# Optimization experiments

Measured on AMD Instinct MI355X. Metric: run time of the kernel, lower is better.

## Reference

```python
import jax, jax.numpy as jnp
import numpy as np

D_MODEL = 128
N_HEADS = 8
N_POINTS = 8
MAX_RES = 10.0


def setup_inputs() -> dict:
    key = jax.random.key(0)
    ks = jax.random.split(key, 12)
    B, C, H, W = 4, D_MODEL, 128, 128
    nh, P = N_HEADS, N_POINTS
    inp = {
        'nbr_fea': jax.random.normal(ks[0], (B, C, H, W), jnp.float32),
        'ext_fea': jax.random.normal(ks[1], (B, C, H, W), jnp.float32),
        'flow': jax.random.normal(ks[2], (B, 2, H, W), jnp.float32) * 2.0,
        'W_off': jax.random.normal(ks[3], (C, nh * P * 2), jnp.float32) * 0.02,
        'b_off': jax.random.normal(ks[4], (nh * P * 2,), jnp.float32) * 0.02,
        'W_attn': jax.random.normal(ks[5], (C, nh * P), jnp.float32) * 0.02,
        'b_attn': jnp.zeros((nh * P,), jnp.float32),
        'W_val': jax.random.normal(ks[6], (C, C), jnp.float32) * (1.0 / np.sqrt(C)),
        'b_val': jnp.zeros((C,), jnp.float32),
        'W_out': jax.random.normal(ks[7], (C, C), jnp.float32) * (1.0 / np.sqrt(C)),
        'b_out': jnp.zeros((C,), jnp.float32),
    }
    return inp


def _bilinear_gather(value, loc, H, W):
    # value: (B, nh, HW, dh)  loc: (B, nh, Q, P, 2) normalized to [0,1]
    # grid_sample semantics: align_corners=False, zero padding
    B, nh, HW, dh = value.shape
    Q, P = loc.shape[2], loc.shape[3]
    x = loc[..., 0] * W - 0.5  # (B,nh,Q,P) pixel coords
    y = loc[..., 1] * H - 0.5
    x0 = jnp.floor(x)
    y0 = jnp.floor(y)
    wx = x - x0
    wy = y - y0
    out = jnp.zeros((B, nh, Q * P, dh), value.dtype)
    for dx, dy, wgt in ((0, 0, (1 - wx) * (1 - wy)), (1, 0, wx * (1 - wy)),
                        (0, 1, (1 - wx) * wy), (1, 1, wx * wy)):
        xi = x0 + dx
        yi = y0 + dy
        valid = (xi >= 0) & (xi < W) & (yi >= 0) & (yi < H)
        xi_c = jnp.clip(xi, 0, W - 1).astype(jnp.int32)
        yi_c = jnp.clip(yi, 0, H - 1).astype(jnp.int32)
        idx = (yi_c * W + xi_c).reshape(B, nh, Q * P, 1)
        g = jnp.take_along_axis(value, idx, axis=2)  # (B,nh,QP,dh)
        w_eff = (wgt * valid.astype(value.dtype)).reshape(B, nh, Q * P, 1)
        out = out + g * w_eff
    return out.reshape(B, nh, Q, P, dh)


def reference(nbr_fea, ext_fea, flow, W_off, b_off, W_attn, b_attn, W_val, b_val, W_out, b_out):
    B, C, H, W = nbr_fea.shape
    nh, P = N_HEADS, N_POINTS
    dh = C // nh
    Q = H * W
    # normalized reference points (pixel centers / extent)
    ys = (jnp.arange(H, dtype=jnp.float32) + 0.5) / H
    xs = (jnp.arange(W, dtype=jnp.float32) + 0.5) / W
    yy, xx = jnp.meshgrid(ys, xs, indexing='ij')
    ref = jnp.stack([xx, yy], -1).reshape(Q, 2)  # (Q,2)

    ext = ext_fea.transpose(0, 2, 3, 1).reshape(B, Q, C)
    # flow-guided sampling offsets (pixels), residue bounded by tanh
    off = MAX_RES * jnp.tanh(ext @ W_off + b_off)
    off = off.reshape(B, Q, nh, P, 2)
    flow_q = flow.transpose(0, 2, 3, 1).reshape(B, Q, 1, 1, 2)
    norm = jnp.array([W, H], jnp.float32)
    loc = ref[None, :, None, None, :] + (flow_q + off) / norm  # (B,Q,nh,P,2)

    attn = jax.nn.softmax((ext @ W_attn + b_attn).reshape(B, Q, nh, P), axis=-1)

    val = (nbr_fea.transpose(0, 2, 3, 1).reshape(B, Q, C) @ W_val + b_val)
    val = val.reshape(B, Q, nh, dh).transpose(0, 2, 1, 3)  # (B,nh,HW,dh)

    sampled = _bilinear_gather(val, loc.transpose(0, 2, 1, 3, 4), H, W)  # (B,nh,Q,P,dh)
    agg = jnp.einsum('bnqpd,bqnp->bqnd', sampled, attn).reshape(B, Q, C)
    out = agg @ W_out + b_out  # (B,Q,C)
    return out.reshape(B, H, W, C).transpose(0, 3, 1, 2)
```

## Files before the change

kernel.cpp:

```cpp
#include <hip/hip_runtime.h>
#include <math.h>

namespace {
constexpr int B   = 4;
constexpr int C   = 128;
constexpr int H   = 128;
constexpr int W   = 128;
constexpr int HWn = H * W;
constexpr int NH  = 8;
}

using short8 = __attribute__((ext_vector_type(8))) short;
using f32x4  = __attribute__((ext_vector_type(4))) float;

__device__ __forceinline__ float fast_tanh(float x) {
  float e = __expf(2.f * x);
  return 1.f - 2.f / (e + 1.f);
}
__device__ __forceinline__ unsigned f2bf(float f) {
  unsigned u = __float_as_uint(f);
  return (u + 0x7FFFu + ((u >> 16) & 1u)) >> 16;
}
__device__ __forceinline__ unsigned pack2bf(float a, float b) {
  return f2bf(a) | (f2bf(b) << 16);
}

__global__ __launch_bounds__(256) void prep_weights_kernel(
    const float* __restrict__ Woff, const float* __restrict__ Wattn,
    const float* __restrict__ Wval, const float* __restrict__ Wout,
    unsigned short* __restrict__ wcat_t, unsigned short* __restrict__ wval_t,
    unsigned short* __restrict__ wout_t) {
  int row = blockIdx.x * 256 + threadIdx.x;
  if (row >= 448) return;
  const float* src; int ldn; int col; unsigned short* dst;
  if (row < 192) {
    if (row < 128) { src = Woff; ldn = 128; col = row; }
    else           { src = Wattn; ldn = 64; col = row - 128; }
    dst = wcat_t + row * 128;
  } else if (row < 320) {
    src = Wval; ldn = 128; col = row - 192; dst = wval_t + (row - 192) * 128;
  } else {
    src = Wout; ldn = 128; col = row - 320; dst = wout_t + (row - 320) * 128;
  }
  for (int k0 = 0; k0 < 128; k0 += 8) {
    unsigned pk[4];
#pragma unroll
    for (int j = 0; j < 4; ++j)
      pk[j] = pack2bf(src[(k0 + 2 * j) * ldn + col],
                      src[(k0 + 2 * j + 1) * ldn + col]);
    *(uint4*)(dst + k0) = make_uint4(pk[0], pk[1], pk[2], pk[3]);
  }
}

__global__ __launch_bounds__(256) void gemm_kernel(
    const float* __restrict__ nbr,
    const unsigned short* __restrict__ wval_t,
    const float* __restrict__ bv,
    unsigned short* __restrict__ val) {
  __shared__ unsigned short a_s[32 * 152];
  const int t    = threadIdx.x;
  const int id   = blockIdx.x;
  const int b    = id >> 9;
  const int q0   = (id & 511) * 32;
  const int wv   = t >> 6;
  const int lane = t & 63;
  const int li   = lane & 15, quad = lane >> 4;

  const float* Ab = nbr + (size_t)b * C * HWn + q0;
#pragma unroll
  for (int it = 0; it < 2; ++it) {
    int idx = t + 256 * it;
    int kp  = idx >> 3;
    int q4  = (idx & 7) * 4;
    float4 fa = *(const float4*)(Ab + (size_t)(2 * kp) * HWn + q4);
    float4 fb = *(const float4*)(Ab + (size_t)(2 * kp + 1) * HWn + q4);
    const float* pa = &fa.x; const float* pb = &fb.x;
#pragma unroll
    for (int j = 0; j < 4; ++j)
      *(unsigned*)&a_s[(q4 + j) * 152 + 2 * kp] = pack2bf(pa[j], pb[j]);
  }
  __syncthreads();

  const int mt = wv & 1;
  const int ng = (wv >> 1) * 4;
  f32x4 acc[4];
#pragma unroll
  for (int i = 0; i < 4; ++i) acc[i] = (f32x4){0.f, 0.f, 0.f, 0.f};

#pragma unroll 1
  for (int ck = 0; ck < 4; ++ck) {
    short8 af = *(const short8*)&a_s[(16 * mt + li) * 152 + ck * 32 + quad * 8];
#pragma unroll
    for (int i = 0; i < 4; ++i) {
      short8 bfr = *(const short8*)(wval_t + (size_t)(16 * (ng + i) + li) * 128 +
                                    ck * 32 + quad * 8);
      acc[i] = __builtin_amdgcn_mfma_f32_16x16x32_bf16(af, bfr, acc[i], 0, 0, 0);
    }
  }
  __syncthreads();

#pragma unroll
  for (int i = 0; i < 4; ++i) {
    int c = 16 * (ng + i) + li;
    float bias = bv[c];
#pragma unroll
    for (int reg = 0; reg < 4; ++reg) {
      int q = mt * 16 + quad * 4 + reg;
      a_s[q * 152 + c] = (unsigned short)f2bf(acc[i][reg] + bias);
    }
  }
  __syncthreads();

  {
    const int qi = t & 31, hs = t >> 5;
    uint4 v0 = *(const uint4*)&a_s[qi * 152 + 16 * hs];
    uint4 v1 = *(const uint4*)&a_s[qi * 152 + 16 * hs + 8];
    unsigned short* d = val + ((size_t)(b * NH + hs) * HWn + q0 + qi) * 16;
    *(uint4*)d = v0; *(uint4*)(d + 8) = v1;
  }
}

__global__ __launch_bounds__(256) void gather_out_kernel(
    const float* __restrict__ flow, const float* __restrict__ ext,
    const unsigned short* __restrict__ wcat_t,
    const float* __restrict__ boff, const float* __restrict__ battn,
    const unsigned short* __restrict__ val,
    const unsigned short* __restrict__ wout_t, const float* __restrict__ bout,
    float* __restrict__ out) {
  __shared__ float smem[32 * 196];
  unsigned short* a_ext = (unsigned short*)smem;
  float* l_s = smem;
  unsigned short* a_s2 = (unsigned short*)smem;
  float* c_s = smem;

  const int t  = threadIdx.x;
  const int qi = t & 31;
  const int r  = t >> 5;

  const int blk  = blockIdx.x;
  const int lin  = (blk & 7) * 256 + (blk >> 3);
  const int b    = lin >> 9;
  const int tile = lin & 511;
  const int x0   = (tile & 7) * 16;
  const int y0   = (tile >> 3) * 2;
  const int x    = x0 + (qi & 15);
  const int y    = y0 + (qi >> 4);

  const int lane = t & 63;
  const int li   = lane & 15, quad = lane >> 4;
  const int wv   = t >> 6;

  {
    const float* Eb = ext + (size_t)b * C * HWn;
#pragma unroll
    for (int it = 0; it < 2; ++it) {
      int idx = t + 256 * it;
      int kp  = idx >> 3;
      int pg  = idx & 7;
      int py  = pg >> 2;
      int xo  = (pg & 3) * 4;
      const float* src = Eb + (size_t)(2 * kp) * HWn + (y0 + py) * W + x0 + xo;
      float4 fa = *(const float4*)src;
      float4 fb = *(const float4*)(src + HWn);
      const float* pa = &fa.x; const float* pb = &fb.x;
#pragma unroll
      for (int j = 0; j < 4; ++j)
        *(unsigned*)&a_ext[(pg * 4 + j) * 136 + 2 * kp] = pack2bf(pa[j], pb[j]);
    }
  }
  __syncthreads();

  {
    const int mt   = wv & 1;
    const int nset = wv >> 1;
    f32x4 lacc[6];
#pragma unroll
    for (int i = 0; i < 6; ++i) lacc[i] = (f32x4){0.f, 0.f, 0.f, 0.f};

#pragma unroll 1
    for (int ks = 0; ks < 4; ++ks) {
      short8 af = *(const short8*)&a_ext[(mt * 16 + li) * 136 + ks * 32 + quad * 8];
#pragma unroll
      for (int i = 0; i < 6; ++i) {
        int n = nset * 6 + i;
        short8 bfr = *(const short8*)(wcat_t + (size_t)(16 * n + li) * 128 +
                                      ks * 32 + quad * 8);
        lacc[i] = __builtin_amdgcn_mfma_f32_16x16x32_bf16(af, bfr, lacc[i], 0, 0, 0);
      }
    }
    __syncthreads();

#pragma unroll
    for (int i = 0; i < 6; ++i) {
      int col = 16 * (nset * 6 + i) + li;
      float bias = (col < 128) ? boff[col] : battn[col - 128];
#pragma unroll
      for (int reg = 0; reg < 4; ++reg) {
        int q = mt * 16 + quad * 4 + reg;
        l_s[q * 196 + col] = lacc[i][reg] + bias;
      }
    }
  }
  __syncthreads();

  const float* lrow = l_s + qi * 196;
  float offa[16];
  float atta[8];
#pragma unroll
  for (int j4 = 0; j4 < 4; ++j4) {
    float4 v = *(const float4*)(lrow + 16 * r + 4 * j4);
    offa[4 * j4 + 0] = 10.f * fast_tanh(v.x);
    offa[4 * j4 + 1] = 10.f * fast_tanh(v.y);
    offa[4 * j4 + 2] = 10.f * fast_tanh(v.z);
    offa[4 * j4 + 3] = 10.f * fast_tanh(v.w);
  }
#pragma unroll
  for (int j4 = 0; j4 < 2; ++j4) {
    float4 v = *(const float4*)(lrow + 128 + 8 * r + 4 * j4);
    atta[4 * j4 + 0] = v.x; atta[4 * j4 + 1] = v.y;
    atta[4 * j4 + 2] = v.z; atta[4 * j4 + 3] = v.w;
  }
  {
    float m = atta[0];
#pragma unroll
    for (int p = 1; p < 8; ++p) m = fmaxf(m, atta[p]);
    float s = 0.f;
#pragma unroll
    for (int p = 0; p < 8; ++p) { float ev = __expf(atta[p] - m); atta[p] = ev; s += ev; }
    float inv = 1.f / s;
#pragma unroll
    for (int p = 0; p < 8; ++p) atta[p] *= inv;
  }
  __syncthreads();

  const float xb = (float)x + flow[(size_t)b * 2 * HWn + y * W + x];
  const float yb = (float)y + flow[((size_t)b * 2 + 1) * HWn + y * W + x];

  float agg[16];
#pragma unroll
  for (int j = 0; j < 16; ++j) agg[j] = 0.f;
  const unsigned short* valh =
      val + ((size_t)b * NH + r) * HWn * 16;

#pragma unroll
  for (int p = 0; p < 8; ++p) {
    float sx = xb + offa[2 * p];
    float sy = yb + offa[2 * p + 1];
    float x0f = floorf(sx), y0f = floorf(sy);
    float wx = sx - x0f, wy = sy - y0f;
    int ix0 = (int)x0f, iy0 = (int)y0f;
    int ix1 = ix0 + 1,  iy1 = iy0 + 1;
    float aw  = atta[p];
    float w00 = aw * (1.f - wx) * (1.f - wy);
    float w10 = aw * wx * (1.f - wy);
    float w01 = aw * (1.f - wx) * wy;
    float w11 = aw * wx * wy;
    if ((unsigned)ix0 >= (unsigned)W) { w00 = 0.f; w01 = 0.f; }
    if ((unsigned)ix1 >= (unsigned)W) { w10 = 0.f; w11 = 0.f; }
    if ((unsigned)iy0 >= (unsigned)H) { w00 = 0.f; w10 = 0.f; }
    if ((unsigned)iy1 >= (unsigned)H) { w01 = 0.f; w11 = 0.f; }
    int x0c = min(max(ix0, 0), W - 1);
    int x1c = min(max(ix1, 0), W - 1);
    int y0c = min(max(iy0, 0), H - 1);
    int y1c = min(max(iy1, 0), H - 1);
    const unsigned short* c00 = valh + (size_t)(y0c * W + x0c) * 16;
    const unsigned short* c10 = valh + (size_t)(y0c * W + x1c) * 16;
    const unsigned short* c01 = valh + (size_t)(y1c * W + x0c) * 16;
    const unsigned short* c11 = valh + (size_t)(y1c * W + x1c) * 16;
#pragma unroll
    for (int cn = 0; cn < 4; ++cn) {
      const unsigned short* cp = (cn == 0) ? c00 : (cn == 1) ? c10
                                : (cn == 2) ? c01 : c11;
      float wgt = (cn == 0) ? w00 : (cn == 1) ? w10 : (cn == 2) ? w01 : w11;
      uint4 ga = ((const uint4*)cp)[0];
      uint4 gb = ((const uint4*)cp)[1];
      unsigned gs[8] = {ga.x, ga.y, ga.z, ga.w, gb.x, gb.y, gb.z, gb.w};
#pragma unroll
      for (int i = 0; i < 8; ++i) {
        float lo = __uint_as_float(gs[i] << 16);
        float hi = __uint_as_float(gs[i] & 0xFFFF0000u);
        agg[2 * i]     += wgt * lo;
        agg[2 * i + 1] += wgt * hi;
      }
    }
  }

  {
    unsigned pk[8];
#pragma unroll
    for (int j = 0; j < 8; ++j) pk[j] = pack2bf(agg[2 * j], agg[2 * j + 1]);
    uint4* dst = (uint4*)&a_s2[qi * 136 + 16 * r];
    dst[0] = make_uint4(pk[0], pk[1], pk[2], pk[3]);
    dst[1] = make_uint4(pk[4], pk[5], pk[6], pk[7]);
  }
  __syncthreads();

  const int mt   = wv & 1;
  const int ng   = (wv >> 1) * 4;

  f32x4 acc[4];
#pragma unroll
  for (int i = 0; i < 4; ++i) acc[i] = (f32x4){0.f, 0.f, 0.f, 0.f};

#pragma unroll 1
  for (int ks = 0; ks < 4; ++ks) {
    short8 af = *(const short8*)&a_s2[(mt * 16 + li) * 136 + ks * 32 + quad * 8];
#pragma unroll
    for (int i = 0; i < 4; ++i) {
      short8 bfr = *(const short8*)(wout_t + (size_t)(16 * (ng + i) + li) * 128 +
                                    ks * 32 + quad * 8);
      acc[i] = __builtin_amdgcn_mfma_f32_16x16x32_bf16(af, bfr, acc[i], 0, 0, 0);
    }
  }
  __syncthreads();

#pragma unroll
  for (int i = 0; i < 4; ++i) {
    int c = 16 * (ng + i) + li;
    float bias = bout[c];
#pragma unroll
    for (int reg = 0; reg < 4; ++reg) {
      int q = mt * 16 + quad * 4 + reg;
      c_s[c * 33 + q] = acc[i][reg] + bias;
    }
  }
  __syncthreads();

  float* ob = out + (size_t)b * C * HWn + y * W + x;
#pragma unroll
  for (int j = 0; j < 16; ++j)
    ob[(size_t)(16 * r + j) * HWn] = c_s[(16 * r + j) * 33 + qi];
}

extern "C" void kernel_launch(void* const* d_in, const int* in_sizes, int n_in,
                              void* d_out, int out_size, void* d_ws, size_t ws_size,
                              hipStream_t stream) {
  const float* nbr   = (const float*)d_in[0];
  const float* extf  = (const float*)d_in[1];
  const float* flow  = (const float*)d_in[2];
  const float* Woff  = (const float*)d_in[3];
  const float* boff  = (const float*)d_in[4];
  const float* Wattn = (const float*)d_in[5];
  const float* battn = (const float*)d_in[6];
  const float* Wval  = (const float*)d_in[7];
  const float* bval  = (const float*)d_in[8];
  const float* Wout  = (const float*)d_in[9];
  const float* bout  = (const float*)d_in[10];
  float* outp = (float*)d_out;

  unsigned short* val    = (unsigned short*)d_ws;
  unsigned short* wcat_t = val + (size_t)B * NH * HWn * 16;
  unsigned short* wval_t = wcat_t + 192 * 128;
  unsigned short* wout_t = wval_t + 128 * 128;

  prep_weights_kernel<<<dim3(2), dim3(256), 0, stream>>>(
      Woff, Wattn, Wval, Wout, wcat_t, wval_t, wout_t);
  gemm_kernel<<<dim3(2048), dim3(256), 0, stream>>>(
      nbr, wval_t, bval, val);
  gather_out_kernel<<<dim3(2048), dim3(256), 0, stream>>>(
      flow, extf, wcat_t, boff, battn, val, wout_t, bout, outp);
}
```

Baseline: 237.7 us.

## Halve gather tile to 16 queries and split head channels across thread halves

The gather/output kernel now processes 16 queries per block instead of 32, and each (query, head) pair is split across two threads that each handle 8 of the 16 head channels. The grid doubles to 4096 blocks, per-thread accumulators and loads shrink, and the MFMA work per wave is reduced to match. This is meant to raise occupancy and memory-level parallelism in the latency-bound bilinear gather. In exchange, the offset/attention math and the per-point bilinear coordinate computation are duplicated across the two channel halves, and the weight loads for the MFMAs are amortized over fewer queries.

```diff
diff --git a/kernel.cpp b/kernel.cpp
--- a/kernel.cpp
+++ b/kernel.cpp
@@ -127,62 +127,53 @@
     const unsigned short* __restrict__ val,
     const unsigned short* __restrict__ wout_t, const float* __restrict__ bout,
     float* __restrict__ out) {
-  __shared__ float smem[32 * 196];
+  __shared__ float smem[16 * 204];
   unsigned short* a_ext = (unsigned short*)smem;
   float* l_s = smem;
   unsigned short* a_s2 = (unsigned short*)smem;
   float* c_s = smem;
 
-  const int t  = threadIdx.x;
-  const int qi = t & 31;
-  const int r  = t >> 5;
+  const int t   = threadIdx.x;
+  const int qi  = t & 15;
+  const int r   = (t >> 4) & 7;
+  const int chh = t >> 7;
 
   const int blk  = blockIdx.x;
-  const int lin  = (blk & 7) * 256 + (blk >> 3);
-  const int b    = lin >> 9;
-  const int tile = lin & 511;
+  const int lin  = (blk & 7) * 512 + (blk >> 3);
+  const int b    = lin >> 10;
+  const int tile = lin & 1023;
   const int x0   = (tile & 7) * 16;
-  const int y0   = (tile >> 3) * 2;
-  const int x    = x0 + (qi & 15);
-  const int y    = y0 + (qi >> 4);
+  const int y    = tile >> 3;
+  const int x    = x0 + qi;
 
   const int lane = t & 63;
   const int li   = lane & 15, quad = lane >> 4;
   const int wv   = t >> 6;
 
   {
-    const float* Eb = ext + (size_t)b * C * HWn;
-#pragma unroll
-    for (int it = 0; it < 2; ++it) {
-      int idx = t + 256 * it;
-      int kp  = idx >> 3;
-      int pg  = idx & 7;
-      int py  = pg >> 2;
-      int xo  = (pg & 3) * 4;
-      const float* src = Eb + (size_t)(2 * kp) * HWn + (y0 + py) * W + x0 + xo;
-      float4 fa = *(const float4*)src;
-      float4 fb = *(const float4*)(src + HWn);
-      const float* pa = &fa.x; const float* pb = &fb.x;
-#pragma unroll
-      for (int j = 0; j < 4; ++j)
-        *(unsigned*)&a_ext[(pg * 4 + j) * 136 + 2 * kp] = pack2bf(pa[j], pb[j]);
-    }
-  }
-  __syncthreads();
-
-  {
-    const int mt   = wv & 1;
-    const int nset = wv >> 1;
-    f32x4 lacc[6];
-#pragma unroll
-    for (int i = 0; i < 6; ++i) lacc[i] = (f32x4){0.f, 0.f, 0.f, 0.f};
+    const float* Eb = ext + (size_t)b * C * HWn + (size_t)y * W + x0;
+    int kp = t >> 2;
+    int xo = (t & 3) * 4;
+    float4 fa = *(const float4*)(Eb + (size_t)(2 * kp) * HWn + xo);
+    float4 fb = *(const float4*)(Eb + (size_t)(2 * kp + 1) * HWn + xo);
+    const float* pa = &fa.x; const float* pb = &fb.x;
+#pragma unroll
+    for (int j = 0; j < 4; ++j)
+      *(unsigned*)&a_ext[(xo + j) * 136 + 2 * kp] = pack2bf(pa[j], pb[j]);
+  }
+  __syncthreads();
+
+  {
+    f32x4 lacc[3];
+#pragma unroll
+    for (int i = 0; i < 3; ++i) lacc[i] = (f32x4){0.f, 0.f, 0.f, 0.f};
 
 #pragma unroll 1
     for (int ks = 0; ks < 4; ++ks) {
-      short8 af = *(const short8*)&a_ext[(mt * 16 + li) * 136 + ks * 32 + quad * 8];
-#pragma unroll
-      for (int i = 0; i < 6; ++i) {
-        int n = nset * 6 + i;
+      short8 af = *(const short8*)&a_ext[li * 136 + ks * 32 + quad * 8];
+#pragma unroll
+      for (int i = 0; i < 3; ++i) {
+        int n = wv * 3 + i;
         short8 bfr = *(const short8*)(wcat_t + (size_t)(16 * n + li) * 128 +
                                       ks * 32 + quad * 8);
         lacc[i] = __builtin_amdgcn_mfma_f32_16x16x32_bf16(af, bfr, lacc[i], 0, 0, 0);
@@ -191,19 +182,19 @@
     __syncthreads();
 
 #pragma unroll
-    for (int i = 0; i < 6; ++i) {
-      int col = 16 * (nset * 6 + i) + li;
+    for (int i = 0; i < 3; ++i) {
+      int col = 16 * (wv * 3 + i) + li;
       float bias = (col < 128) ? boff[col] : battn[col - 128];
 #pragma unroll
       for (int reg = 0; reg < 4; ++reg) {
-        int q = mt * 16 + quad * 4 + reg;
-        l_s[q * 196 + col] = lacc[i][reg] + bias;
+        int q = quad * 4 + reg;
+        l_s[q * 204 + col] = lacc[i][reg] + bias;
       }
     }
   }
   __syncthreads();
 
-  const float* lrow = l_s + qi * 196;
+  const float* lrow = l_s + qi * 204;
   float offa[16];
   float atta[8];
 #pragma unroll
@@ -236,11 +227,11 @@
   const float xb = (float)x + flow[(size_t)b * 2 * HWn + y * W + x];
   const float yb = (float)y + flow[((size_t)b * 2 + 1) * HWn + y * W + x];
 
-  float agg[16];
-#pragma unroll
-  for (int j = 0; j < 16; ++j) agg[j] = 0.f;
+  float agg[8];
+#pragma unroll
+  for (int j = 0; j < 8; ++j) agg[j] = 0.f;
   const unsigned short* valh =
-      val + ((size_t)b * NH + r) * HWn * 16;
+      val + ((size_t)b * NH + r) * HWn * 16 + 8 * chh;
 
 #pragma unroll
   for (int p = 0; p < 8; ++p) {
@@ -272,11 +263,10 @@
       const unsigned short* cp = (cn == 0) ? c00 : (cn == 1) ? c10
                                 : (cn == 2) ? c01 : c11;
       float wgt = (cn == 0) ? w00 : (cn == 1) ? w10 : (cn == 2) ? w01 : w11;
-      uint4 ga = ((const uint4*)cp)[0];
-      uint4 gb = ((const uint4*)cp)[1];
-      unsigned gs[8] = {ga.x, ga.y, ga.z, ga.w, gb.x, gb.y, gb.z, gb.w};
-#pragma unroll
-      for (int i = 0; i < 8; ++i) {
+      uint4 ga = *(const uint4*)cp;
+      unsigned gs[4] = {ga.x, ga.y, ga.z, ga.w};
+#pragma unroll
+      for (int i = 0; i < 4; ++i) {
         float lo = __uint_as_float(gs[i] << 16);
         float hi = __uint_as_float(gs[i] & 0xFFFF0000u);
         agg[2 * i]     += wgt * lo;
@@ -286,27 +276,24 @@
   }
 
   {
-    unsigned pk[8];
-#pragma unroll
-    for (int j = 0; j < 8; ++j) pk[j] = pack2bf(agg[2 * j], agg[2 * j + 1]);
-    uint4* dst = (uint4*)&a_s2[qi * 136 + 16 * r];
-    dst[0] = make_uint4(pk[0], pk[1], pk[2], pk[3]);
-    dst[1] = make_uint4(pk[4], pk[5], pk[6], pk[7]);
-  }
-  __syncthreads();
-
-  const int mt   = wv & 1;
-  const int ng   = (wv >> 1) * 4;
-
-  f32x4 acc[4];
-#pragma unroll
-  for (int i = 0; i < 4; ++i) acc[i] = (f32x4){0.f, 0.f, 0.f, 0.f};
+    unsigned pk[4];
+#pragma unroll
+    for (int j = 0; j < 4; ++j) pk[j] = pack2bf(agg[2 * j], agg[2 * j + 1]);
+    *(uint4*)&a_s2[qi * 136 + 16 * r + 8 * chh] =
+        make_uint4(pk[0], pk[1], pk[2], pk[3]);
+  }
+  __syncthreads();
+
+  const int ng = wv * 2;
+  f32x4 acc[2];
+#pragma unroll
+  for (int i = 0; i < 2; ++i) acc[i] = (f32x4){0.f, 0.f, 0.f, 0.f};
 
 #pragma unroll 1
   for (int ks = 0; ks < 4; ++ks) {
-    short8 af = *(const short8*)&a_s2[(mt * 16 + li) * 136 + ks * 32 + quad * 8];
-#pragma unroll
-    for (int i = 0; i < 4; ++i) {
+    short8 af = *(const short8*)&a_s2[li * 136 + ks * 32 + quad * 8];
+#pragma unroll
+    for (int i = 0; i < 2; ++i) {
       short8 bfr = *(const short8*)(wout_t + (size_t)(16 * (ng + i) + li) * 128 +
                                     ks * 32 + quad * 8);
       acc[i] = __builtin_amdgcn_mfma_f32_16x16x32_bf16(af, bfr, acc[i], 0, 0, 0);
@@ -315,21 +302,23 @@
   __syncthreads();
 
 #pragma unroll
-  for (int i = 0; i < 4; ++i) {
+  for (int i = 0; i < 2; ++i) {
     int c = 16 * (ng + i) + li;
     float bias = bout[c];
 #pragma unroll
     for (int reg = 0; reg < 4; ++reg) {
-      int q = mt * 16 + quad * 4 + reg;
-      c_s[c * 33 + q] = acc[i][reg] + bias;
-    }
-  }
-  __syncthreads();
-
-  float* ob = out + (size_t)b * C * HWn + y * W + x;
-#pragma unroll
-  for (int j = 0; j < 16; ++j)
-    ob[(size_t)(16 * r + j) * HWn] = c_s[(16 * r + j) * 33 + qi];
+      int q = quad * 4 + reg;
+      c_s[c * 17 + q] = acc[i][reg] + bias;
+    }
+  }
+  __syncthreads();
+
+  float* ob = out + (size_t)b * C * HWn + (size_t)y * W + x;
+#pragma unroll
+  for (int j = 0; j < 8; ++j) {
+    int cc = 16 * r + 8 * chh + j;
+    ob[(size_t)cc * HWn] = c_s[cc * 17 + qi];
+  }
 }
 
 extern "C" void kernel_launch(void* const* d_in, const int* in_sizes, int n_in,
@@ -357,6 +346,6 @@
       Woff, Wattn, Wval, Wout, wcat_t, wval_t, wout_t);
   gemm_kernel<<<dim3(2048), dim3(256), 0, stream>>>(
       nbr, wval_t, bval, val);
-  gather_out_kernel<<<dim3(2048), dim3(256), 0, stream>>>(
+  gather_out_kernel<<<dim3(4096), dim3(256), 0, stream>>>(
       flow, extf, wcat_t, boff, battn, val, wout_t, bout, outp);
 }
```

Result: no change. 236.0 us (-0.7%).

## Move offset/attention projection into the GEMM kernel and stage it in global memory

Applied to the files above, without the earlier changes.

The ext-feature projection (offsets and attention logits) moves out of the gather kernel into the first GEMM kernel as a second group of blocks. Those blocks write fp32 results to a workspace buffer, and the gather kernel reads them back per query. This lightens the gather kernel (less shared memory, fewer syncs, likely higher occupancy) and lets the projection run in parallel with the value GEMM. The cost is an extra round-trip of about 50 MB of fp32 projection data through global memory.

```diff
diff --git a/kernel.cpp b/kernel.cpp
--- a/kernel.cpp
+++ b/kernel.cpp
@@ -24,6 +24,7 @@
 __device__ __forceinline__ unsigned pack2bf(float a, float b) {
   return f2bf(a) | (f2bf(b) << 16);
 }
+
 
 __global__ __launch_bounds__(256) void prep_weights_kernel(
     const float* __restrict__ Woff, const float* __restrict__ Wattn,
@@ -53,20 +54,23 @@
 }
 
 __global__ __launch_bounds__(256) void gemm_kernel(
-    const float* __restrict__ nbr,
+    const float* __restrict__ nbr, const float* __restrict__ ext,
     const unsigned short* __restrict__ wval_t,
     const float* __restrict__ bv,
-    unsigned short* __restrict__ val) {
+    const unsigned short* __restrict__ wcat_t,
+    const float* __restrict__ boff, const float* __restrict__ battn,
+    unsigned short* __restrict__ val, float* __restrict__ proj) {
   __shared__ unsigned short a_s[32 * 152];
   const int t    = threadIdx.x;
-  const int id   = blockIdx.x;
+  const int grp  = blockIdx.x >> 11;
+  const int id   = blockIdx.x & 2047;
   const int b    = id >> 9;
   const int q0   = (id & 511) * 32;
   const int wv   = t >> 6;
   const int lane = t & 63;
   const int li   = lane & 15, quad = lane >> 4;
 
-  const float* Ab = nbr + (size_t)b * C * HWn + q0;
+  const float* Ab = (grp ? ext : nbr) + (size_t)b * C * HWn + q0;
 #pragma unroll
   for (int it = 0; it < 2; ++it) {
     int idx = t + 256 * it;
@@ -82,54 +86,81 @@
   __syncthreads();
 
   const int mt = wv & 1;
-  const int ng = (wv >> 1) * 4;
-  f32x4 acc[4];
-#pragma unroll
-  for (int i = 0; i < 4; ++i) acc[i] = (f32x4){0.f, 0.f, 0.f, 0.f};
+
+  if (grp == 0) {
+    const int ng = (wv >> 1) * 4;
+    f32x4 acc[4];
+#pragma unroll
+    for (int i = 0; i < 4; ++i) acc[i] = (f32x4){0.f, 0.f, 0.f, 0.f};
 
 #pragma unroll 1
-  for (int ck = 0; ck < 4; ++ck) {
-    short8 af = *(const short8*)&a_s[(16 * mt + li) * 152 + ck * 32 + quad * 8];
+    for (int ck = 0; ck < 4; ++ck) {
+      short8 af = *(const short8*)&a_s[(16 * mt + li) * 152 + ck * 32 + quad * 8];
+#pragma unroll
+      for (int i = 0; i < 4; ++i) {
+        short8 bfr = *(const short8*)(wval_t + (size_t)(16 * (ng + i) + li) * 128 +
+                                      ck * 32 + quad * 8);
+        acc[i] = __builtin_amdgcn_mfma_f32_16x16x32_bf16(af, bfr, acc[i], 0, 0, 0);
+      }
+    }
+    __syncthreads();
+
 #pragma unroll
     for (int i = 0; i < 4; ++i) {
-      short8 bfr = *(const short8*)(wval_t + (size_t)(16 * (ng + i) + li) * 128 +
-                                    ck * 32 + quad * 8);
-      acc[i] = __builtin_amdgcn_mfma_f32_16x16x32_bf16(af, bfr, acc[i], 0, 0, 0);
-    }
-  }
-  __syncthreads();
-
-#pragma unroll
-  for (int i = 0; i < 4; ++i) {
-    int c = 16 * (ng + i) + li;
-    float bias = bv[c];
-#pragma unroll
-    for (int reg = 0; reg < 4; ++reg) {
-      int q = mt * 16 + quad * 4 + reg;
-      a_s[q * 152 + c] = (unsigned short)f2bf(acc[i][reg] + bias);
-    }
-  }
-  __syncthreads();
-
-  {
-    const int qi = t & 31, hs = t >> 5;
-    uint4 v0 = *(const uint4*)&a_s[qi * 152 + 16 * hs];
-    uint4 v1 = *(const uint4*)&a_s[qi * 152 + 16 * hs + 8];
-    unsigned short* d = val + ((size_t)(b * NH + hs) * HWn + q0 + qi) * 16;
-    *(uint4*)d = v0; *(uint4*)(d + 8) = v1;
+      int c = 16 * (ng + i) + li;
+      float bias = bv[c];
+#pragma unroll
+      for (int reg = 0; reg < 4; ++reg) {
+        int q = mt * 16 + quad * 4 + reg;
+        a_s[q * 152 + c] = (unsigned short)f2bf(acc[i][reg] + bias);
+      }
+    }
+    __syncthreads();
+
+    {
+      const int qi = t & 31, hs = t >> 5;
+      uint4 v0 = *(const uint4*)&a_s[qi * 152 + 16 * hs];
+      uint4 v1 = *(const uint4*)&a_s[qi * 152 + 16 * hs + 8];
+      unsigned short* d = val + ((size_t)(b * NH + hs) * HWn + q0 + qi) * 16;
+      *(uint4*)d = v0; *(uint4*)(d + 8) = v1;
+    }
+  } else {
+    const int nset = wv >> 1;
+    f32x4 lacc[6];
+#pragma unroll
+    for (int i = 0; i < 6; ++i) lacc[i] = (f32x4){0.f, 0.f, 0.f, 0.f};
+
+#pragma unroll 1
+    for (int ck = 0; ck < 4; ++ck) {
+      short8 af = *(const short8*)&a_s[(16 * mt + li) * 152 + ck * 32 + quad * 8];
+#pragma unroll
+      for (int i = 0; i < 6; ++i) {
+        int n = nset * 6 + i;
+        short8 bfr = *(const short8*)(wcat_t + (size_t)(16 * n + li) * 128 +
+                                      ck * 32 + quad * 8);
+        lacc[i] = __builtin_amdgcn_mfma_f32_16x16x32_bf16(af, bfr, lacc[i], 0, 0, 0);
+      }
+    }
+
+#pragma unroll
+    for (int i = 0; i < 6; ++i) {
+      int col = 16 * (nset * 6 + i) + li;
+      float bias = (col < 128) ? boff[col] : battn[col - 128];
+#pragma unroll
+      for (int reg = 0; reg < 4; ++reg) {
+        int q = mt * 16 + quad * 4 + reg;
+        proj[(size_t)(b * HWn + q0 + q) * 192 + col] = lacc[i][reg] + bias;
+      }
+    }
   }
 }
 
 __global__ __launch_bounds__(256) void gather_out_kernel(
-    const float* __restrict__ flow, const float* __restrict__ ext,
-    const unsigned short* __restrict__ wcat_t,
-    const float* __restrict__ boff, const float* __restrict__ battn,
+    const float* __restrict__ flow, const float* __restrict__ proj,
     const unsigned short* __restrict__ val,
     const unsigned short* __restrict__ wout_t, const float* __restrict__ bout,
     float* __restrict__ out) {
-  __shared__ float smem[32 * 196];
-  unsigned short* a_ext = (unsigned short*)smem;
-  float* l_s = smem;
+  __shared__ float smem[128 * 33];
   unsigned short* a_s2 = (unsigned short*)smem;
   float* c_s = smem;
 
@@ -146,69 +177,12 @@
   const int x    = x0 + (qi & 15);
   const int y    = y0 + (qi >> 4);
 
-  const int lane = t & 63;
-  const int li   = lane & 15, quad = lane >> 4;
-  const int wv   = t >> 6;
-
-  {
-    const float* Eb = ext + (size_t)b * C * HWn;
-#pragma unroll
-    for (int it = 0; it < 2; ++it) {
-      int idx = t + 256 * it;
-      int kp  = idx >> 3;
-      int pg  = idx & 7;
-      int py  = pg >> 2;
-      int xo  = (pg & 3) * 4;
-      const float* src = Eb + (size_t)(2 * kp) * HWn + (y0 + py) * W + x0 + xo;
-      float4 fa = *(const float4*)src;
-      float4 fb = *(const float4*)(src + HWn);
-      const float* pa = &fa.x; const float* pb = &fb.x;
-#pragma unroll
-      for (int j = 0; j < 4; ++j)
-        *(unsigned*)&a_ext[(pg * 4 + j) * 136 + 2 * kp] = pack2bf(pa[j], pb[j]);
-    }
-  }
-  __syncthreads();
-
-  {
-    const int mt   = wv & 1;
-    const int nset = wv >> 1;
-    f32x4 lacc[6];
-#pragma unroll
-    for (int i = 0; i < 6; ++i) lacc[i] = (f32x4){0.f, 0.f, 0.f, 0.f};
-
-#pragma unroll 1
-    for (int ks = 0; ks < 4; ++ks) {
-      short8 af = *(const short8*)&a_ext[(mt * 16 + li) * 136 + ks * 32 + quad * 8];
-#pragma unroll
-      for (int i = 0; i < 6; ++i) {
-        int n = nset * 6 + i;
-        short8 bfr = *(const short8*)(wcat_t + (size_t)(16 * n + li) * 128 +
-                                      ks * 32 + quad * 8);
-        lacc[i] = __builtin_amdgcn_mfma_f32_16x16x32_bf16(af, bfr, lacc[i], 0, 0, 0);
-      }
-    }
-    __syncthreads();
-
-#pragma unroll
-    for (int i = 0; i < 6; ++i) {
-      int col = 16 * (nset * 6 + i) + li;
-      float bias = (col < 128) ? boff[col] : battn[col - 128];
-#pragma unroll
-      for (int reg = 0; reg < 4; ++reg) {
-        int q = mt * 16 + quad * 4 + reg;
-        l_s[q * 196 + col] = lacc[i][reg] + bias;
-      }
-    }
-  }
-  __syncthreads();
-
-  const float* lrow = l_s + qi * 196;
+  const float* pp = proj + (size_t)(b * HWn + y * W + x) * 192;
   float offa[16];
   float atta[8];
 #pragma unroll
   for (int j4 = 0; j4 < 4; ++j4) {
-    float4 v = *(const float4*)(lrow + 16 * r + 4 * j4);
+    float4 v = *(const float4*)(pp + 16 * r + 4 * j4);
     offa[4 * j4 + 0] = 10.f * fast_tanh(v.x);
     offa[4 * j4 + 1] = 10.f * fast_tanh(v.y);
     offa[4 * j4 + 2] = 10.f * fast_tanh(v.z);
@@ -216,7 +190,7 @@
   }
 #pragma unroll
   for (int j4 = 0; j4 < 2; ++j4) {
-    float4 v = *(const float4*)(lrow + 128 + 8 * r + 4 * j4);
+    float4 v = *(const float4*)(pp + 128 + 8 * r + 4 * j4);
     atta[4 * j4 + 0] = v.x; atta[4 * j4 + 1] = v.y;
     atta[4 * j4 + 2] = v.z; atta[4 * j4 + 3] = v.w;
   }
@@ -231,7 +205,6 @@
 #pragma unroll
     for (int p = 0; p < 8; ++p) atta[p] *= inv;
   }
-  __syncthreads();
 
   const float xb = (float)x + flow[(size_t)b * 2 * HWn + y * W + x];
   const float yb = (float)y + flow[((size_t)b * 2 + 1) * HWn + y * W + x];
@@ -295,6 +268,9 @@
   }
   __syncthreads();
 
+  const int lane = t & 63;
+  const int li   = lane & 15, quad = lane >> 4;
+  const int wv   = t >> 6;
   const int mt   = wv & 1;
   const int ng   = (wv >> 1) * 4;
 
@@ -352,11 +328,12 @@
   unsigned short* wcat_t = val + (size_t)B * NH * HWn * 16;
   unsigned short* wval_t = wcat_t + 192 * 128;
   unsigned short* wout_t = wval_t + 128 * 128;
+  float*          proj   = (float*)(wout_t + 128 * 128);
 
   prep_weights_kernel<<<dim3(2), dim3(256), 0, stream>>>(
       Woff, Wattn, Wval, Wout, wcat_t, wval_t, wout_t);
-  gemm_kernel<<<dim3(2048), dim3(256), 0, stream>>>(
-      nbr, wval_t, bval, val);
+  gemm_kernel<<<dim3(4096), dim3(256), 0, stream>>>(
+      nbr, extf, wval_t, bval, wcat_t, boff, battn, val, proj);
   gather_out_kernel<<<dim3(2048), dim3(256), 0, stream>>>(
-      flow, extf, wcat_t, boff, battn, val, wout_t, bout, outp);
-}
+      flow, proj, val, wout_t, bout, outp);
+}
```

After: 248.1 us. 1.04x slower.
